# Optimization experiments

Hardware: AMD Instinct MI355X
Metric: run time of the kernel (lower is better)

Reference implementation:

```python
import jax, jax.numpy as jnp
import numpy as np

THRESH = 6.0   # latent_dist_threshold
SCALE = 1.0    # reward_scale
EPS = 1e-6


def _count_scatter(idx, vals):
    # idx, vals: [B, V, N]; counts[b,v,s] = sum of vals over queries whose argmin == s
    B, V, N = idx.shape
    bi = jnp.arange(B)[:, None, None]
    vi = jnp.arange(V)[None, :, None]
    return jnp.zeros((B, V, N), jnp.int32).at[bi, vi, idx].add(vals)


def _direction(min_dists, min_idx, query_xy, source_xy, query_mask):
    # one chamfer direction: queries matched to nearest source particles
    d = jnp.take_along_axis(source_xy, min_idx[..., None], axis=2)  # [B,V,N,2]
    dist = jnp.linalg.norm(query_xy - d, ord=2, axis=-1)            # [B,V,N]
    latent_mask = min_dists > THRESH
    rpm = query_mask | latent_mask                                   # reward_particle_mask
    vals = jnp.where(rpm, 0, 1).astype(jnp.int32)
    count = _count_scatter(min_idx, vals)                            # density counts per source
    w = 1.0 / (jnp.take_along_axis(count, min_idx, axis=2).astype(jnp.float32) + EPS)
    dist = jnp.where(rpm, 0.0, w * dist)
    unmatched = jnp.any((~query_mask) & latent_mask, axis=-1).astype(jnp.float32)
    groups = jnp.maximum(jnp.sum(count > 0, axis=2).astype(jnp.float32) + unmatched, 1.0)
    return -(jnp.sum(dist, axis=2) + unmatched) / groups             # [B,V]


def setup_inputs() -> dict:
    key = jax.random.key(0)
    k1, k2 = jax.random.split(key)
    achieved = jax.random.normal(k1, (256, 2, 512, 10), dtype=jnp.float32)
    desired = jax.random.normal(k2, (256, 2, 512, 10), dtype=jnp.float32)
    return {"achieved": achieved, "desired": desired}


def reference(achieved, desired):
    # latent_classifier=None -> obj_class_cond = ones -> mask = (ones == 0) = all False
    state_mask = jnp.zeros(achieved.shape[:-1], bool)
    goal_mask = jnp.zeros(desired.shape[:-1], bool)
    s_vis = achieved[..., 5:9]
    s_xy = achieved[..., :2]
    g_vis = desired[..., 5:9]
    g_xy = desired[..., :2]
    # 'l2_simple' pairwise squared dist: P[b,v,i,j] = ||s_vis_i - g_vis_j||^2
    P = (jnp.sum(s_vis ** 2, -1)[..., :, None]
         + jnp.sum(g_vis ** 2, -1)[..., None, :]
         - 2.0 * jnp.einsum('bvnd,bvmd->bvnm', s_vis, g_vis))
    P = jnp.where(state_mask[..., :, None] | goal_mask[..., None, :], jnp.inf, P)
    # goal -> state: min over state axis (2)
    md1 = jnp.min(P, axis=2)
    mi1 = jnp.argmin(P, axis=2).astype(jnp.int32)
    r_g2s = _direction(md1, mi1, g_xy, s_xy, goal_mask)
    # state -> goal: min over goal axis (3)
    md2 = jnp.min(P, axis=3)
    mi2 = jnp.argmin(P, axis=3).astype(jnp.int32)
    r_s2g = _direction(md2, mi2, s_xy, g_xy, state_mask)
    rv = (r_g2s + r_s2g) / 2.0                                       # [B,V]
    no_valid = jnp.all(goal_mask, -1) | jnp.all(state_mask, -1)
    rv = jnp.where(no_valid, -1.0, rv)
    reward = jnp.mean(rv, axis=1)
    return SCALE * reward[:, None]                                    # [B,1]
```

## Files before the change

kernel.cpp:

```cpp
#include <hip/hip_runtime.h>
#include <math.h>

#define NB 256
#define NV 2
#define NN 512
#define ND 10
#define THRESH_SQ 6.0f
#define EPS_W 1e-6f

typedef __attribute__((ext_vector_type(8))) short bf16x8;
typedef __attribute__((ext_vector_type(4))) float f32x4;

__device__ __forceinline__ unsigned short f2bf(float x) {
    union { float f; unsigned u; } v; v.f = x;
    unsigned r = v.u + 0x7FFFu + ((v.u >> 16) & 1u);
    return (unsigned short)(r >> 16);
}
__device__ __forceinline__ float bf2f(unsigned short h) {
    union { unsigned u; float f; } v; v.u = ((unsigned)h) << 16; return v.f;
}
__device__ __forceinline__ void split3(float x, unsigned short* s) {
    unsigned short h = f2bf(x); float r = x - bf2f(h);
    unsigned short m = f2bf(r); float r2 = r - bf2f(m);
    s[0] = h; s[1] = m; s[2] = f2bf(r2);
}
__device__ __forceinline__ unsigned umin_(unsigned a, unsigned b) { return a < b ? a : b; }

__device__ __forceinline__ int recaddr(int c, int row) {
    return (c << 13) + ((row << 4) ^ (c << 5));
}

__global__ __launch_bounds__(512, 6)
void chamfer_bv(const float* __restrict__ achieved,
                const float* __restrict__ desired,
                float* __restrict__ rv_out)
{
    const int bv  = blockIdx.x;
    const int tid = threadIdx.x;

    __shared__ __align__(16) char buf[32768];
    __shared__ unsigned colKey[NN * 2];

    const float* arow = achieved + ((size_t)bv * NN + tid) * ND;
    const float* drow = desired  + ((size_t)bv * NN + tid) * ND;

    const unsigned short ONE = 0x3F80;
    const int pi[6] = {0,0,1,2,1,0};
    const int pj[6] = {0,1,0,0,1,2};

    const float g5 = drow[5], g6 = drow[6], g7 = drow[7], g8 = drow[8];

    {
        float a5 = arow[5], a6 = arow[6], a7 = arow[7], a8 = arow[8];
        unsigned short us[4][3];
        split3(-2.0f*a5, us[0]); split3(-2.0f*a6, us[1]);
        split3(-2.0f*a7, us[2]); split3(-2.0f*a8, us[3]);
        float sn2 = a5*a5 + a6*a6 + a7*a7 + a8*a8;
        unsigned short sn[3]; split3(sn2, sn);
        unsigned short t[32];
        #pragma unroll
        for (int d = 0; d < 4; ++d)
            #pragma unroll
            for (int p = 0; p < 6; ++p)
                t[d*6+p] = us[d][pi[p]];
        t[24]=sn[0]; t[25]=sn[1]; t[26]=sn[2];
        t[27]=ONE;   t[28]=ONE;   t[29]=ONE;
        t[30]=ONE;   t[31]=0;
        #pragma unroll
        for (int c = 0; c < 4; ++c) {
            bf16x8 v;
            #pragma unroll
            for (int e = 0; e < 8; ++e) v[e] = (short)t[c*8+e];
            *(bf16x8*)(buf + recaddr(c, tid)) = v;
        }
    }
    colKey[tid*2]   = 0xFFFFFFFFu;
    colKey[tid*2+1] = 0xFFFFFFFFu;
    __syncthreads();

    const int lane = tid & 63, wid = tid >> 6;
    const int lrow = lane & 15, lchk = lane >> 4;

    bf16x8 afr[4];
    #pragma unroll
    for (int nt = 0; nt < 4; ++nt)
        afr[nt] = *(const bf16x8*)(buf + recaddr(lchk, (wid<<6) + (nt<<4) + lrow));
    __syncthreads();

    {
        unsigned short gs[4][3];
        split3(g5, gs[0]); split3(g6, gs[1]); split3(g7, gs[2]); split3(g8, gs[3]);
        float gn2 = g5*g5 + g6*g6 + g7*g7 + g8*g8;
        unsigned short gn[3]; split3(gn2, gn);
        unsigned short t[32];
        #pragma unroll
        for (int d = 0; d < 4; ++d)
            #pragma unroll
            for (int p = 0; p < 6; ++p)
                t[d*6+p] = gs[d][pj[p]];
        t[24]=ONE;   t[25]=ONE;   t[26]=ONE;
        t[27]=gn[0]; t[28]=gn[1]; t[29]=gn[2];
        t[30]=0x3A80; t[31]=0;
        #pragma unroll
        for (int c = 0; c < 4; ++c) {
            bf16x8 v;
            #pragma unroll
            for (int e = 0; e < 8; ++e) v[e] = (short)t[c*8+e];
            *(bf16x8*)(buf + recaddr(c, tid)) = v;
        }
    }
    __syncthreads();

    unsigned rowKey[4][4];
    int ncst[4][4];
    #pragma unroll
    for (int nt = 0; nt < 4; ++nt)
        #pragma unroll
        for (int j = 0; j < 4; ++j) {
            rowKey[nt][j] = 0xFFFFFFFFu;
            ncst[nt][j]   = (wid<<6) + (nt<<4) + (lchk<<2) + j;
        }

    const unsigned MASK = 0xFFFFFE00u;
    const f32x4 z = {0.0f, 0.0f, 0.0f, 0.0f};
    const int cslice = lchk >> 1;

    #pragma unroll 4
    for (int mt = 0; mt < 32; ++mt) {
        bf16x8 bfr = *(const bf16x8*)(buf + recaddr(lchk, (mt<<4) + lrow));
        const unsigned mcur = (unsigned)((mt<<4) + lrow);
        unsigned cv = 0xFFFFFFFFu;
        #pragma unroll
        for (int nt = 0; nt < 4; ++nt) {
            f32x4 acc = __builtin_amdgcn_mfma_f32_16x16x32_bf16(afr[nt], bfr, z, 0, 0, 0);
            #pragma unroll
            for (int j = 0; j < 4; ++j) {
                unsigned bits = __float_as_uint(acc[j]);
                rowKey[nt][j] = umin_(rowKey[nt][j], (bits & MASK) | mcur);
                cv = umin_(cv, (bits & MASK) | (unsigned)ncst[nt][j]);
            }
        }
        atomicMin(&colKey[(mcur << 1) | cslice], cv);
    }

    #pragma unroll
    for (int nt = 0; nt < 4; ++nt) {
        #pragma unroll
        for (int j = 0; j < 4; ++j) {
            unsigned v = rowKey[nt][j];
            #pragma unroll
            for (int s = 1; s <= 8; s <<= 1)
                v = umin_(v, (unsigned)__shfl_xor((int)v, s));
            rowKey[nt][j] = v;
        }
    }
    __syncthreads();

    unsigned* rowKeyArr = (unsigned*)buf;
    int*      cnt       = (int*)(buf + 2048);
    float*    redF      = (float*)(buf + 4096);
    int*      redI      = (int*)(buf + 4160);

    if (lrow == 0) {
        #pragma unroll
        for (int nt = 0; nt < 4; ++nt)
            #pragma unroll
            for (int j = 0; j < 4; ++j)
                rowKeyArr[ncst[nt][j]] = rowKey[nt][j];
    }
    cnt[tid] = 0;
    __syncthreads();

    const unsigned kA = umin_(colKey[tid*2], colKey[tid*2+1]);
    const unsigned kB = rowKeyArr[tid];
    const int miA = (int)(kA & 0x1FFu);
    const int miB = (int)(kB & 0x1FFu);
    const bool latA = __uint_as_float(kA & MASK) > THRESH_SQ;
    const bool latB = __uint_as_float(kB & MASK) > THRESH_SQ;
    if (!latA) atomicAdd(&cnt[miA], 1);
    if (!latB) atomicAdd(&cnt[miB], 0x10000);
    __syncthreads();

    float sumA = 0.0f, sumB = 0.0f;
    if (!latA) {
        const float* sp = achieved + ((size_t)bv * NN + miA) * ND;
        float dx = drow[0] - sp[0], dy = drow[1] - sp[1];
        float w = 1.0f / ((float)(cnt[miA] & 0xFFFF) + EPS_W);
        sumA = w * sqrtf(dx*dx + dy*dy);
    }
    if (!latB) {
        const float* gp = desired + ((size_t)bv * NN + miB) * ND;
        float dx = arow[0] - gp[0], dy = arow[1] - gp[1];
        float w = 1.0f / ((float)(((unsigned)cnt[miB]) >> 16) + EPS_W);
        sumB = w * sqrtf(dx*dx + dy*dy);
    }
    const int c0 = cnt[tid];
    int grpPk = ((c0 & 0xFFFF) ? 1 : 0) | ((((unsigned)c0) >> 16) ? 0x10000 : 0);
    int latPk = (latA ? 1 : 0) | (latB ? 2 : 0);

    #pragma unroll
    for (int off = 32; off > 0; off >>= 1) {
        sumA  += __shfl_down(sumA, off);
        sumB  += __shfl_down(sumB, off);
        grpPk += __shfl_down(grpPk, off);
        latPk |= __shfl_down(latPk, off);
    }
    if (lane == 0) {
        redF[wid*2] = sumA; redF[wid*2+1] = sumB;
        redI[wid*2] = grpPk; redI[wid*2+1] = latPk;
    }
    __syncthreads();
    if (tid == 0) {
        float sA = 0.0f, sB = 0.0f; int G = 0, L = 0;
        #pragma unroll
        for (int w2 = 0; w2 < 8; ++w2) {
            sA += redF[w2*2]; sB += redF[w2*2+1];
            G  += redI[w2*2]; L |= redI[w2*2+1];
        }
        float unmA = (L & 1) ? 1.0f : 0.0f;
        float unmB = (L & 2) ? 1.0f : 0.0f;
        float gA = (float)(G & 0xFFFF), gB = (float)(((unsigned)G) >> 16);
        float rA = -(sA + unmA) / fmaxf(gA + unmA, 1.0f);
        float rB = -(sB + unmB) / fmaxf(gB + unmB, 1.0f);
        rv_out[bv] = 0.5f * (rA + rB);
    }
}

__global__ void chamfer_finalize(const float* __restrict__ rv, float* __restrict__ out)
{
    int b = blockIdx.x * 256 + threadIdx.x;
    if (b < NB) out[b] = 0.5f * (rv[2*b] + rv[2*b + 1]);
}

extern "C" void kernel_launch(void* const* d_in, const int* in_sizes, int n_in,
                              void* d_out, int out_size, void* d_ws, size_t ws_size,
                              hipStream_t stream)
{
    const float* achieved = (const float*)d_in[0];
    const float* desired  = (const float*)d_in[1];
    float* out = (float*)d_out;
    float* rv  = (float*)d_ws;

    chamfer_bv<<<NB * NV, 512, 0, stream>>>(achieved, desired, rv);
    chamfer_finalize<<<1, 256, 0, stream>>>(rv, out);
}
```

Measured before the change: 30.68 us.

## Replace LDS atomicMin column reduction with a second transposed MFMA pass

New measurement: 36.29 us. 18.3% more time.

```diff
diff --git a/kernel.cpp b/kernel.cpp
--- a/kernel.cpp
+++ b/kernel.cpp
@@ -30,7 +30,7 @@
     return (c << 13) + ((row << 4) ^ (c << 5));
 }
 
-__global__ __launch_bounds__(512, 6)
+__global__ __launch_bounds__(512, 4)
 void chamfer_bv(const float* __restrict__ achieved,
                 const float* __restrict__ desired,
                 float* __restrict__ rv_out)
@@ -38,8 +38,7 @@
     const int bv  = blockIdx.x;
     const int tid = threadIdx.x;
 
-    __shared__ __align__(16) char buf[32768];
-    __shared__ unsigned colKey[NN * 2];
+    __shared__ __align__(16) char lds[65536];
 
     const float* arow = achieved + ((size_t)bv * NN + tid) * ND;
     const float* drow = desired  + ((size_t)bv * NN + tid) * ND;
@@ -71,22 +70,9 @@
             bf16x8 v;
             #pragma unroll
             for (int e = 0; e < 8; ++e) v[e] = (short)t[c*8+e];
-            *(bf16x8*)(buf + recaddr(c, tid)) = v;
-        }
-    }
-    colKey[tid*2]   = 0xFFFFFFFFu;
-    colKey[tid*2+1] = 0xFFFFFFFFu;
-    __syncthreads();
-
-    const int lane = tid & 63, wid = tid >> 6;
-    const int lrow = lane & 15, lchk = lane >> 4;
-
-    bf16x8 afr[4];
-    #pragma unroll
-    for (int nt = 0; nt < 4; ++nt)
-        afr[nt] = *(const bf16x8*)(buf + recaddr(lchk, (wid<<6) + (nt<<4) + lrow));
-    __syncthreads();
-
+            *(bf16x8*)(lds + recaddr(c, tid)) = v;
+        }
+    }
     {
         unsigned short gs[4][3];
         split3(g5, gs[0]); split3(g6, gs[1]); split3(g7, gs[2]); split3(g8, gs[3]);
@@ -106,41 +92,53 @@
             bf16x8 v;
             #pragma unroll
             for (int e = 0; e < 8; ++e) v[e] = (short)t[c*8+e];
-            *(bf16x8*)(buf + recaddr(c, tid)) = v;
-        }
-    }
-    __syncthreads();
-
-    unsigned rowKey[4][4];
-    int ncst[4][4];
-    #pragma unroll
-    for (int nt = 0; nt < 4; ++nt)
-        #pragma unroll
-        for (int j = 0; j < 4; ++j) {
-            rowKey[nt][j] = 0xFFFFFFFFu;
-            ncst[nt][j]   = (wid<<6) + (nt<<4) + (lchk<<2) + j;
-        }
+            *(bf16x8*)(lds + 32768 + recaddr(c, tid)) = v;
+        }
+    }
+    __syncthreads();
+
+    const int lane = tid & 63, wid = tid >> 6;
+    const int lrow = lane & 15, lchk = lane >> 4;
 
     const unsigned MASK = 0xFFFFFE00u;
     const f32x4 z = {0.0f, 0.0f, 0.0f, 0.0f};
-    const int cslice = lchk >> 1;
-
-    #pragma unroll 4
-    for (int mt = 0; mt < 32; ++mt) {
-        bf16x8 bfr = *(const bf16x8*)(buf + recaddr(lchk, (mt<<4) + lrow));
-        const unsigned mcur = (unsigned)((mt<<4) + lrow);
-        unsigned cv = 0xFFFFFFFFu;
-        #pragma unroll
-        for (int nt = 0; nt < 4; ++nt) {
-            f32x4 acc = __builtin_amdgcn_mfma_f32_16x16x32_bf16(afr[nt], bfr, z, 0, 0, 0);
-            #pragma unroll
-            for (int j = 0; j < 4; ++j) {
-                unsigned bits = __float_as_uint(acc[j]);
-                rowKey[nt][j] = umin_(rowKey[nt][j], (bits & MASK) | mcur);
-                cv = umin_(cv, (bits & MASK) | (unsigned)ncst[nt][j]);
+
+    int slotIdx[4][4];
+    #pragma unroll
+    for (int nt = 0; nt < 4; ++nt)
+        #pragma unroll
+        for (int j = 0; j < 4; ++j)
+            slotIdx[nt][j] = (wid<<6) + (nt<<4) + (lchk<<2) + j;
+
+    bf16x8 afr[4];
+    #pragma unroll
+    for (int nt = 0; nt < 4; ++nt)
+        afr[nt] = *(const bf16x8*)(lds + recaddr(lchk, (wid<<6) + (nt<<4) + lrow));
+
+    unsigned rowKey[4][4];
+    #pragma unroll
+    for (int nt = 0; nt < 4; ++nt)
+        #pragma unroll
+        for (int j = 0; j < 4; ++j) rowKey[nt][j] = 0xFFFFFFFFu;
+
+    {
+        bf16x8 bfr = *(const bf16x8*)(lds + 32768 + recaddr(lchk, lrow));
+        #pragma unroll 4
+        for (int mt = 0; mt < 32; ++mt) {
+            const int mtn = (mt + 1) & 31;
+            bf16x8 bnext = *(const bf16x8*)(lds + 32768 + recaddr(lchk, (mtn<<4) + lrow));
+            const unsigned mcur = (unsigned)((mt<<4) + lrow);
+            #pragma unroll
+            for (int nt = 0; nt < 4; ++nt) {
+                f32x4 acc = __builtin_amdgcn_mfma_f32_16x16x32_bf16(afr[nt], bfr, z, 0, 0, 0);
+                #pragma unroll
+                for (int j = 0; j < 4; ++j) {
+                    unsigned k = (__float_as_uint(acc[j]) & MASK) | mcur;
+                    rowKey[nt][j] = umin_(rowKey[nt][j], k);
+                }
             }
-        }
-        atomicMin(&colKey[(mcur << 1) | cslice], cv);
+            bfr = bnext;
+        }
     }
 
     #pragma unroll
@@ -154,24 +152,78 @@
             rowKey[nt][j] = v;
         }
     }
-    __syncthreads();
-
-    unsigned* rowKeyArr = (unsigned*)buf;
-    int*      cnt       = (int*)(buf + 2048);
-    float*    redF      = (float*)(buf + 4096);
-    int*      redI      = (int*)(buf + 4160);
-
+
+    bf16x8 afr2[4];
+    #pragma unroll
+    for (int nt = 0; nt < 4; ++nt)
+        afr2[nt] = *(const bf16x8*)(lds + 32768 + recaddr(lchk, (wid<<6) + (nt<<4) + lrow));
+
+    __syncthreads();
+
+    unsigned* rowKeyArr = (unsigned*)(lds + 32768);
     if (lrow == 0) {
         #pragma unroll
         for (int nt = 0; nt < 4; ++nt)
             #pragma unroll
             for (int j = 0; j < 4; ++j)
-                rowKeyArr[ncst[nt][j]] = rowKey[nt][j];
+                rowKeyArr[slotIdx[nt][j]] = rowKey[nt][j];
+    }
+
+    unsigned colKey[4][4];
+    #pragma unroll
+    for (int nt = 0; nt < 4; ++nt)
+        #pragma unroll
+        for (int j = 0; j < 4; ++j) colKey[nt][j] = 0xFFFFFFFFu;
+
+    {
+        bf16x8 bfr = *(const bf16x8*)(lds + recaddr(lchk, lrow));
+        #pragma unroll 4
+        for (int nt2 = 0; nt2 < 32; ++nt2) {
+            const int ntn = (nt2 + 1) & 31;
+            bf16x8 bnext = *(const bf16x8*)(lds + recaddr(lchk, (ntn<<4) + lrow));
+            const unsigned ncur = (unsigned)((nt2<<4) + lrow);
+            #pragma unroll
+            for (int nt = 0; nt < 4; ++nt) {
+                f32x4 acc = __builtin_amdgcn_mfma_f32_16x16x32_bf16(afr2[nt], bfr, z, 0, 0, 0);
+                #pragma unroll
+                for (int j = 0; j < 4; ++j) {
+                    unsigned k = (__float_as_uint(acc[j]) & MASK) | ncur;
+                    colKey[nt][j] = umin_(colKey[nt][j], k);
+                }
+            }
+            bfr = bnext;
+        }
+    }
+
+    #pragma unroll
+    for (int nt = 0; nt < 4; ++nt) {
+        #pragma unroll
+        for (int j = 0; j < 4; ++j) {
+            unsigned v = colKey[nt][j];
+            #pragma unroll
+            for (int s = 1; s <= 8; s <<= 1)
+                v = umin_(v, (unsigned)__shfl_xor((int)v, s));
+            colKey[nt][j] = v;
+        }
+    }
+    __syncthreads();
+
+    unsigned* colKeyArr = (unsigned*)lds;
+    int*      cnt       = (int*)(lds + 2048);
+    float*    redF      = (float*)(lds + 4096);
+    int*      redI      = (int*)(lds + 4160);
+
+    if (lrow == 0) {
+        #pragma unroll
+        for (int nt = 0; nt < 4; ++nt)
+            #pragma unroll
+            for (int j = 0; j < 4; ++j)
+                colKeyArr[slotIdx[nt][j]] = colKey[nt][j];
     }
     cnt[tid] = 0;
     __syncthreads();
 
-    const unsigned kA = umin_(colKey[tid*2], colKey[tid*2+1]);
+    const unsigned kA = colKeyArr[tid];
     const unsigned kB = rowKeyArr[tid];
     const int miA = (int)(kA & 0x1FFu);
     const int miB = (int)(kB & 0x1FFu);
```
